# Performance work log

Measured on AMD Instinct MI355X. Metric: run time of the kernel, lower is better.

## Reference

```python
import jax, jax.numpy as jnp
import numpy as np

STALENESS_LAMBDA = 0.001
TEMPERATURE = 1.0
TOP_K = 3
EPS = 1e-8


def setup_inputs() -> dict:
    key = jax.random.key(0)
    ks = jax.random.split(key, 6)
    B, D, H, E = 131072, 512, 256, 10
    features = jax.random.normal(ks[0], (B, D), dtype=jnp.float32)
    W_proj = jax.random.normal(ks[1], (D, H), dtype=jnp.float32) * 0.02
    b_proj = jnp.zeros((H,), dtype=jnp.float32)
    expert_emb = jax.random.normal(ks[2], (E, H), dtype=jnp.float32) * 0.01
    expert_features = jax.random.normal(ks[3], (E, D), dtype=jnp.float32)
    trust = jax.random.uniform(ks[4], (E,), dtype=jnp.float32)
    delta_t = jax.random.uniform(ks[5], (E,), dtype=jnp.float32) * 100.0
    return {"features": features, "W_proj": W_proj, "b_proj": b_proj,
            "expert_emb": expert_emb, "expert_features": expert_features,
            "trust": trust, "delta_t": delta_t}


def reference(features, W_proj, b_proj, expert_emb, expert_features, trust, delta_t):
    H = W_proj.shape[1]
    # learned gate: sigmoid(proj(x) . e_j / sqrt(H))  -> (B, E)
    proj = features @ W_proj + b_proj                                  # (B, H)
    gate = jax.nn.sigmoid(jnp.einsum('bh,eh->be', proj, expert_emb)
                          / jnp.sqrt(jnp.float32(H)))
    # cosine similarity S_ij mapped to [0, 1]                          # (B, E)
    fn = features / jnp.maximum(jnp.linalg.norm(features, axis=1, keepdims=True), EPS)
    en = expert_features / jnp.maximum(
        jnp.linalg.norm(expert_features, axis=1, keepdims=True), EPS)
    sim = (jnp.einsum('bd,ed->be', fn, en) + 1.0) * 0.5
    # staleness decay e^{-lambda * dt} and base score T*S*decay
    stale = jnp.exp(-STALENESS_LAMBDA * delta_t)                        # (E,)
    score = gate * (trust * stale)[None, :] * sim                       # (B, E)
    probs = jax.nn.softmax(score / TEMPERATURE, axis=-1)                # (B, E)
    topk_w, topk_idx = jax.lax.top_k(probs, TOP_K)                      # (B, K)
    topk_w = topk_w / jnp.sum(topk_w, axis=-1, keepdims=True)
    return topk_w, topk_idx, probs
```

## Files before the change

kernel.cpp:

```cpp
#include <hip/hip_runtime.h>
#include <stdint.h>
#include <math.h>

#define D_DIM 512
#define H_DIM 256
#define E_NUM 10

typedef float f16v __attribute__((ext_vector_type(16)));

__global__ __launch_bounds__(256) void pre_wg(const float* __restrict__ Wp,
                                              const float* __restrict__ bp,
                                              const float* __restrict__ emb,
                                              float* __restrict__ pk,
                                              float* __restrict__ bg) {
  int gid = blockIdx.x * 256 + threadIdx.x;
  if (gid < E_NUM * D_DIM) {
    int d = gid / E_NUM;
    int e = gid - d * E_NUM;
    const float* wr = Wp + (size_t)d * H_DIM;
    const float* er = emb + (size_t)e * H_DIM;
    float s0 = 0.f, s1 = 0.f, s2 = 0.f, s3 = 0.f;
#pragma unroll 4
    for (int h = 0; h < H_DIM; h += 4) {
      float4 a = *(const float4*)(wr + h);
      float4 b = *(const float4*)(er + h);
      s0 = fmaf(a.x, b.x, s0); s1 = fmaf(a.y, b.y, s1);
      s2 = fmaf(a.z, b.z, s2); s3 = fmaf(a.w, b.w, s3);
    }
    pk[(size_t)(d >> 2) * 80 + e * 8 + (d & 3)] = ((s0 + s1) + (s2 + s3)) * 0.0625f;
  } else if (gid < E_NUM * D_DIM + E_NUM) {
    int e = gid - E_NUM * D_DIM;
    const float* er = emb + (size_t)e * H_DIM;
    float s = 0.f;
    for (int h = 0; h < H_DIM; ++h) s = fmaf(bp[h], er[h], s);
    bg[e] = s * 0.0625f;
  }
}

__global__ __launch_bounds__(64) void pre_en(const float* __restrict__ ef,
                                             const float* __restrict__ trust,
                                             const float* __restrict__ dtv,
                                             float* __restrict__ pk,
                                             float* __restrict__ cf) {
  int e = blockIdx.x, l = threadIdx.x;
  const float* row = ef + (size_t)e * D_DIM;
  float s = 0.f;
#pragma unroll
  for (int j = 0; j < D_DIM / 64; ++j) { float v = row[l + 64 * j]; s = fmaf(v, v, s); }
#pragma unroll
  for (int o = 32; o; o >>= 1) s += __shfl_xor(s, o, 64);
  float inv = 1.f / fmaxf(sqrtf(s), 1e-8f);
#pragma unroll
  for (int j = 0; j < D_DIM / 64; ++j) {
    int d = l + 64 * j;
    pk[(size_t)(d >> 2) * 80 + e * 8 + 4 + (d & 3)] = row[d] * inv;
  }
  if (l == 0) cf[e] = trust[e] * expf(-0.001f * dtv[e]);
}

#define WV(i) ((i) < 16 ? w0[(i) & 15] : (i) < 32 ? w1[(i) & 15] : \
               (i) < 48 ? w2[(i) & 15] : (i) < 64 ? w3[(i) & 15] : w4[(i) & 15])

__global__ __launch_bounds__(256, 4) void router_main(
    const float* __restrict__ feat, const float* __restrict__ pk,
    const float* __restrict__ cf, const float* __restrict__ bg,
    float* __restrict__ out, int B) {
  __shared__ float red[3 * 64 * 23];
  const int t = threadIdx.x;
  const int l = t & 63;
  const int w = __builtin_amdgcn_readfirstlane(t >> 6);
  const size_t row = (size_t)blockIdx.x * 64 + l;
  const float* gp = feat + row * D_DIM + w * 128;
  const float* wq = pk + (size_t)w * 32 * 80;

  float acc[21];
#pragma unroll
  for (int i = 0; i < 21; ++i) acc[i] = 0.f;

  float4 fvA[8], fvB[8];
#pragma unroll
  for (int j = 0; j < 8; ++j) fvA[j] = *(const float4*)(gp + j * 4);

#pragma unroll
  for (int it = 0; it < 4; ++it) {
    float4* cur = (it & 1) ? fvB : fvA;
    float4* nxt = (it & 1) ? fvA : fvB;
    if (it < 3) {
#pragma unroll
      for (int j = 0; j < 8; ++j) nxt[j] = *(const float4*)(gp + (it + 1) * 32 + j * 4);
    }
#pragma unroll
    for (int sub = 0; sub < 8; ++sub) {
      f16v w0, w1, w2, w3, w4;
      const float* wp = wq + (it * 8 + sub) * 80;
      asm volatile(
          "s_load_dwordx16 %0, %5, 0x0\n"
          "s_load_dwordx16 %1, %5, 0x40\n"
          "s_load_dwordx16 %2, %5, 0x80\n"
          "s_load_dwordx16 %3, %5, 0xc0\n"
          "s_load_dwordx16 %4, %5, 0x100\n"
          "s_waitcnt lgkmcnt(0)"
          : "=&s"(w0), "=&s"(w1), "=&s"(w2), "=&s"(w3), "=&s"(w4)
          : "s"(wp));
      float4 f = cur[sub];
#pragma unroll
      for (int e = 0; e < E_NUM; ++e) {
        const int b = e * 8;
        float a = acc[e];
        a = fmaf(f.x, WV(b + 0), a); a = fmaf(f.y, WV(b + 1), a);
        a = fmaf(f.z, WV(b + 2), a); a = fmaf(f.w, WV(b + 3), a);
        acc[e] = a;
        float s2 = acc[10 + e];
        s2 = fmaf(f.x, WV(b + 4), s2); s2 = fmaf(f.y, WV(b + 5), s2);
        s2 = fmaf(f.z, WV(b + 6), s2); s2 = fmaf(f.w, WV(b + 7), s2);
        acc[10 + e] = s2;
      }
      float n = acc[20];
      n = fmaf(f.x, f.x, n); n = fmaf(f.y, f.y, n);
      n = fmaf(f.z, f.z, n); n = fmaf(f.w, f.w, n);
      acc[20] = n;
    }
  }

  if (w) {
    float* rp = &red[((w - 1) * 64 + l) * 23];
#pragma unroll
    for (int i = 0; i < 21; ++i) rp[i] = acc[i];
  }
  __syncthreads();
  if (w == 0) {
#pragma unroll
    for (int s = 0; s < 3; ++s) {
      const float* rp = &red[(s * 64 + l) * 23];
#pragma unroll
      for (int i = 0; i < 21; ++i) acc[i] += rp[i];
    }

    const float inv = 1.f / fmaxf(sqrtf(acc[20]), 1e-8f);
    float probs[E_NUM];
    float m = -1e30f;
#pragma unroll
    for (int e = 0; e < E_NUM; ++e) {
      float logit = acc[e] + bg[e];
      float gate = 1.f / (1.f + __expf(-logit));
      float sim = fmaf(acc[10 + e] * inv, 0.5f, 0.5f);
      float sc = gate * cf[e] * sim;
      probs[e] = sc;
      m = fmaxf(m, sc);
    }
    float Z = 0.f;
#pragma unroll
    for (int e = 0; e < E_NUM; ++e) { float pe = __expf(probs[e] - m); probs[e] = pe; Z += pe; }
    const float invZ = 1.f / Z;
#pragma unroll
    for (int e = 0; e < E_NUM; ++e) probs[e] *= invZ;

    int i0 = 0; float b0 = probs[0];
#pragma unroll
    for (int e = 1; e < E_NUM; ++e) if (probs[e] > b0) { b0 = probs[e]; i0 = e; }
    int i1 = -1; float b1 = -1.f;
#pragma unroll
    for (int e = 0; e < E_NUM; ++e) if (e != i0 && probs[e] > b1) { b1 = probs[e]; i1 = e; }
    int i2 = -1; float b2 = -1.f;
#pragma unroll
    for (int e = 0; e < E_NUM; ++e) if (e != i0 && e != i1 && probs[e] > b2) { b2 = probs[e]; i2 = e; }

    const float wnorm = 1.f / (b0 + b1 + b2);
    float* ow = out + row * 3;
    ow[0] = b0 * wnorm; ow[1] = b1 * wnorm; ow[2] = b2 * wnorm;
    float* oi = out + (size_t)B * 3 + row * 3;
    oi[0] = (float)i0; oi[1] = (float)i1; oi[2] = (float)i2;
    float* op = out + (size_t)B * 6 + row * E_NUM;
#pragma unroll
    for (int e = 0; e < E_NUM; ++e) op[e] = probs[e];
  }
}

extern "C" void kernel_launch(void* const* d_in, const int* in_sizes, int n_in,
                              void* d_out, int out_size, void* d_ws, size_t ws_size,
                              hipStream_t stream) {
  const float* feat  = (const float*)d_in[0];
  const float* Wp    = (const float*)d_in[1];
  const float* bp    = (const float*)d_in[2];
  const float* emb   = (const float*)d_in[3];
  const float* ef    = (const float*)d_in[4];
  const float* trust = (const float*)d_in[5];
  const float* dtv   = (const float*)d_in[6];
  float* out = (float*)d_out;

  float* pk = (float*)d_ws;
  float* cf = pk + 128 * 80;
  float* bg = cf + E_NUM;

  const int B = in_sizes[0] / D_DIM;

  hipLaunchKernelGGL(pre_wg, dim3((E_NUM * D_DIM + E_NUM + 255) / 256), dim3(256),
                     0, stream, Wp, bp, emb, pk, bg);
  hipLaunchKernelGGL(pre_en, dim3(E_NUM), dim3(64), 0, stream, ef, trust, dtv, pk, cf);
  hipLaunchKernelGGL(router_main, dim3(B / 64), dim3(256), 0, stream,
                     feat, pk, cf, bg, out, B);
}
```

Measured before the change: 81.16 us.

## Use packed FP32 FMA with per-d weight layout and raise occupancy

Repacks the precomputed weights so each feature dimension stores 20 contiguous gate and similarity coefficients, letting the inner loop issue packed two-wide FMAs (v_pk_fma_f32) over expert pairs. It halves the prefetch buffer depth (4 float4 per stage instead of 8) and raises launch bounds to 6 waves per SIMD to improve latency hiding on this bandwidth-bound pass over the features. The risks are register spills under the tighter bound and scalar-load waits that are now less well hidden, since each scalar weight load covers fewer FMAs.

```diff
diff --git a/kernel.cpp b/kernel.cpp
--- a/kernel.cpp
+++ b/kernel.cpp
@@ -7,6 +7,7 @@
 #define E_NUM 10
 
 typedef float f16v __attribute__((ext_vector_type(16)));
+typedef float f2 __attribute__((ext_vector_type(2)));
 
 __global__ __launch_bounds__(256) void pre_wg(const float* __restrict__ Wp,
                                               const float* __restrict__ bp,
@@ -27,7 +28,7 @@
       s0 = fmaf(a.x, b.x, s0); s1 = fmaf(a.y, b.y, s1);
       s2 = fmaf(a.z, b.z, s2); s3 = fmaf(a.w, b.w, s3);
     }
-    pk[(size_t)(d >> 2) * 80 + e * 8 + (d & 3)] = ((s0 + s1) + (s2 + s3)) * 0.0625f;
+    pk[(size_t)d * 20 + e] = ((s0 + s1) + (s2 + s3)) * 0.0625f;
   } else if (gid < E_NUM * D_DIM + E_NUM) {
     int e = gid - E_NUM * D_DIM;
     const float* er = emb + (size_t)e * H_DIM;
@@ -53,15 +54,15 @@
 #pragma unroll
   for (int j = 0; j < D_DIM / 64; ++j) {
     int d = l + 64 * j;
-    pk[(size_t)(d >> 2) * 80 + e * 8 + 4 + (d & 3)] = row[d] * inv;
+    pk[(size_t)d * 20 + 10 + e] = row[d] * inv;
   }
   if (l == 0) cf[e] = trust[e] * expf(-0.001f * dtv[e]);
 }
 
-#define WV(i) ((i) < 16 ? w0[(i) & 15] : (i) < 32 ? w1[(i) & 15] : \
-               (i) < 48 ? w2[(i) & 15] : (i) < 64 ? w3[(i) & 15] : w4[(i) & 15])
-
-__global__ __launch_bounds__(256, 4) void router_main(
+#define WVx(i) ((i) < 16 ? w0[(i) & 15] : (i) < 32 ? w1[(i) & 15] : \
+                (i) < 48 ? w2[(i) & 15] : (i) < 64 ? w3[(i) & 15] : w4[(i) & 15])
+
+__global__ __launch_bounds__(256, 6) void router_main(
     const float* __restrict__ feat, const float* __restrict__ pk,
     const float* __restrict__ cf, const float* __restrict__ bg,
     float* __restrict__ out, int B) {
@@ -71,28 +72,29 @@
   const int w = __builtin_amdgcn_readfirstlane(t >> 6);
   const size_t row = (size_t)blockIdx.x * 64 + l;
   const float* gp = feat + row * D_DIM + w * 128;
-  const float* wq = pk + (size_t)w * 32 * 80;
-
-  float acc[21];
-#pragma unroll
-  for (int i = 0; i < 21; ++i) acc[i] = 0.f;
-
-  float4 fvA[8], fvB[8];
-#pragma unroll
-  for (int j = 0; j < 8; ++j) fvA[j] = *(const float4*)(gp + j * 4);
-
-#pragma unroll
-  for (int it = 0; it < 4; ++it) {
+  const float* wq = pk + (size_t)w * 128 * 20;
+
+  f2 ag[5], as_[5], n2;
+#pragma unroll
+  for (int i = 0; i < 5; ++i) { ag[i] = f2{0.f, 0.f}; as_[i] = f2{0.f, 0.f}; }
+  n2 = f2{0.f, 0.f};
+
+  float4 fvA[4], fvB[4];
+#pragma unroll
+  for (int j = 0; j < 4; ++j) fvA[j] = *(const float4*)(gp + j * 4);
+
+#pragma unroll
+  for (int it = 0; it < 8; ++it) {
     float4* cur = (it & 1) ? fvB : fvA;
     float4* nxt = (it & 1) ? fvA : fvB;
-    if (it < 3) {
-#pragma unroll
-      for (int j = 0; j < 8; ++j) nxt[j] = *(const float4*)(gp + (it + 1) * 32 + j * 4);
-    }
-#pragma unroll
-    for (int sub = 0; sub < 8; ++sub) {
+    if (it < 7) {
+#pragma unroll
+      for (int j = 0; j < 4; ++j) nxt[j] = *(const float4*)(gp + (it + 1) * 16 + j * 4);
+    }
+#pragma unroll
+    for (int sub = 0; sub < 4; ++sub) {
       f16v w0, w1, w2, w3, w4;
-      const float* wp = wq + (it * 8 + sub) * 80;
+      const float* wp = wq + (it * 4 + sub) * 80;
       asm volatile(
           "s_load_dwordx16 %0, %5, 0x0\n"
           "s_load_dwordx16 %1, %5, 0x40\n"
@@ -104,23 +106,32 @@
           : "s"(wp));
       float4 f = cur[sub];
 #pragma unroll
-      for (int e = 0; e < E_NUM; ++e) {
-        const int b = e * 8;
-        float a = acc[e];
-        a = fmaf(f.x, WV(b + 0), a); a = fmaf(f.y, WV(b + 1), a);
-        a = fmaf(f.z, WV(b + 2), a); a = fmaf(f.w, WV(b + 3), a);
-        acc[e] = a;
-        float s2 = acc[10 + e];
-        s2 = fmaf(f.x, WV(b + 4), s2); s2 = fmaf(f.y, WV(b + 5), s2);
-        s2 = fmaf(f.z, WV(b + 6), s2); s2 = fmaf(f.w, WV(b + 7), s2);
-        acc[10 + e] = s2;
+      for (int q = 0; q < 4; ++q) {
+        const float fq = (q == 0) ? f.x : (q == 1) ? f.y : (q == 2) ? f.z : f.w;
+        const f2 fq2 = {fq, fq};
+#pragma unroll
+        for (int j = 0; j < 5; ++j) {
+          const int bgi = q * 20 + 2 * j;
+          f2 wg2 = {WVx(bgi), WVx(bgi + 1)};
+          ag[j] = __builtin_elementwise_fma(fq2, wg2, ag[j]);
+        }
+#pragma unroll
+        for (int j = 0; j < 5; ++j) {
+          const int bsi = q * 20 + 10 + 2 * j;
+          f2 ws2 = {WVx(bsi), WVx(bsi + 1)};
+          as_[j] = __builtin_elementwise_fma(fq2, ws2, as_[j]);
+        }
       }
-      float n = acc[20];
-      n = fmaf(f.x, f.x, n); n = fmaf(f.y, f.y, n);
-      n = fmaf(f.z, f.z, n); n = fmaf(f.w, f.w, n);
-      acc[20] = n;
-    }
-  }
+      f2 p0 = {f.x, f.y}, p1 = {f.z, f.w};
+      n2 = __builtin_elementwise_fma(p0, p0, n2);
+      n2 = __builtin_elementwise_fma(p1, p1, n2);
+    }
+  }
+
+  float acc[21];
+#pragma unroll
+  for (int e = 0; e < E_NUM; ++e) { acc[e] = ag[e >> 1][e & 1]; acc[10 + e] = as_[e >> 1][e & 1]; }
+  acc[20] = n2.x + n2.y;
 
   if (w) {
     float* rp = &red[((w - 1) * 64 + l) * 23];
@@ -189,7 +200,7 @@
   float* out = (float*)d_out;
 
   float* pk = (float*)d_ws;
-  float* cf = pk + 128 * 80;
+  float* cf = pk + D_DIM * 20;
   float* bg = cf + E_NUM;
 
   const int B = in_sizes[0] / D_DIM;
```

New measurement: 73.68 us. -9.2%, faster.
